# Kernel optimization log

Measured on AMD Instinct MI355X. Metric: run time of the kernel, lower is better.

The kernel has to match this reference:

```python
import jax, jax.numpy as jnp
import numpy as np

PAD_TOKEN_ID = 0
PAGE_SIZE = 64
BOUNDARY_IDS = (13, 30)


def setup_inputs() -> dict:
    B, L, V = 64, 16384, 32000
    P = L // PAGE_SIZE
    key = jax.random.key(0)
    k1, k2, k3 = jax.random.split(key, 3)
    input_ids = jax.random.randint(k1, (B, L), 0, V, dtype=jnp.int32)
    attention_mask = jnp.ones((B, L), dtype=jnp.int32)
    # token -> page index, exactly pos // page_size as SegmentPager would build
    token2page = jnp.broadcast_to(jnp.arange(L, dtype=jnp.int32) // PAGE_SIZE, (B, L))
    keep_pages = jax.random.bernoulli(k2, 0.3, (B, P))  # bool [B, P]
    query_pos = jax.random.randint(k3, (B,), 0, L, dtype=jnp.int32)
    return {
        'input_ids': input_ids,
        'attention_mask': attention_mask,
        'token2page': token2page,
        'keep_pages': keep_pages,
        'query_pos': query_pos,
    }


def reference(input_ids, attention_mask, token2page, keep_pages, query_pos):
    B, L = input_ids.shape
    valid = attention_mask.astype(bool)                         # token_valid [B,L]
    pos = jnp.arange(L, dtype=jnp.int32)

    # --- page-level keep mask gathered per token ---
    t2p = jnp.clip(token2page, 0, None)
    page_keep = jnp.take_along_axis(keep_pages, t2p, axis=1)    # [B,L] bool
    mask = valid & page_keep                                    # keep_token

    # --- force-keep the query tail: mask[qp:] |= valid[qp:] ---
    qp = jnp.clip(query_pos.astype(jnp.int32), 0, L - 1)        # [B]
    tail = pos[None, :] >= qp[:, None]
    mask = mask | (tail & valid)

    # --- sentence rescue in context [0, qp): if any token of a sentence is kept,
    #     keep all valid tokens of that sentence. Sentences are delimited by
    #     boundary tokens (segment = exclusive cumsum of boundary indicators). ---
    boundary = jnp.zeros_like(valid)
    for tid in BOUNDARY_IDS:
        boundary = boundary | (input_ids == tid)
    boundary = boundary & valid
    bcnt = boundary.astype(jnp.int32)
    seg = jnp.cumsum(bcnt, axis=1) - bcnt                       # sentence id per token
    in_ctx = pos[None, :] < qp[:, None]
    seg_d = jnp.where(in_ctx, seg, L)                           # dummy segment L for non-ctx
    flat_seg = (jnp.arange(B, dtype=jnp.int32)[:, None] * (L + 1) + seg_d).reshape(-1)
    keep_any = jax.ops.segment_max(mask.astype(jnp.int32).reshape(-1), flat_seg,
                                   num_segments=B * (L + 1))
    tok_keep = (keep_any[flat_seg] > 0).reshape(B, L)
    mask = mask | (in_ctx & valid & tok_keep)

    # --- fallback: if nothing kept, keep last valid token (or position 0) ---
    any_kept = mask.any(axis=1)
    any_valid = valid.any(axis=1)
    last_valid = jnp.where(any_valid, L - 1 - jnp.argmax(valid[:, ::-1], axis=1), 0)
    fallback = pos[None, :] == last_valid[:, None]
    mask = jnp.where(any_kept[:, None], mask, fallback)

    # --- stream compaction + left-justified padding (padded to L for static shape) ---
    order = jnp.argsort(jnp.logical_not(mask), axis=1)          # stable: kept indices first, in order
    lk = mask.sum(axis=1).astype(jnp.int32)                     # kept length per row
    attn = pos[None, :] < lk[:, None]
    ids_sorted = jnp.take_along_axis(input_ids, order, axis=1)
    ids_comp = jnp.where(attn, ids_sorted, PAD_TOKEN_ID)
    attn_comp = attn.astype(jnp.int32)
    pos_comp = jnp.where(attn, pos[None, :], 0)
    return ids_comp, attn_comp, pos_comp
```

## Files before the change

kernel.cpp:

```cpp
#include <hip/hip_runtime.h>
#include <stdint.h>

#define BB 64
#define LL 16384
#define PP 256
#define WW (LL / 32)
#define NT2 512

__global__ void __launch_bounds__(256) k1_masks(
    const int* __restrict__ g_ids, const int* __restrict__ g_amask,
    const int* __restrict__ g_t2p, const int* __restrict__ g_kp,
    const int* __restrict__ g_qp,
    unsigned* __restrict__ validw, unsigned* __restrict__ bndw,
    unsigned* __restrict__ mask1w)
{
    __shared__ unsigned char kp[PP];
    const int chunk = blockIdx.x;
    const int row   = blockIdx.y;
    const int t     = threadIdx.x;
    if (t < PP) kp[t] = (g_kp[row * PP + t] != 0);
    int qp = g_qp[row];
    qp = qp < 0 ? 0 : (qp > LL - 1 ? LL - 1 : qp);
    __syncthreads();

    const int pos0 = chunk * 2048 + t * 8;
    const int g = row * LL + pos0;
    const int4* idp = (const int4*)(g_ids + g);
    const int4* amp = (const int4*)(g_amask + g);
    const int4* tpp = (const int4*)(g_t2p + g);
    unsigned v8 = 0, b8 = 0, m8 = 0;
#pragma unroll
    for (int jv = 0; jv < 2; ++jv) {
        int4 iv = idp[jv], av = amp[jv], pv = tpp[jv];
        int idsv[4] = {iv.x, iv.y, iv.z, iv.w};
        int amv[4]  = {av.x, av.y, av.z, av.w};
        int tpv[4]  = {pv.x, pv.y, pv.z, pv.w};
#pragma unroll
        for (int k = 0; k < 4; ++k) {
            const int j = jv * 4 + k;
            const int va = (amv[k] != 0);
            const int bd = va && (idsv[k] == 13 || idsv[k] == 30);
            int pg = tpv[k];
            pg = pg < 0 ? 0 : (pg > PP - 1 ? PP - 1 : pg);
            const int m1 = va && (kp[pg] || (pos0 + j) >= qp);
            v8 |= (unsigned)va << j;
            b8 |= (unsigned)bd << j;
            m8 |= (unsigned)m1 << j;
        }
    }
    const int sub = t & 3, sh = 8 * sub;
    unsigned vw = v8 << sh, bw = b8 << sh, mw = m8 << sh;
    vw |= __shfl_xor(vw, 1, 64); vw |= __shfl_xor(vw, 2, 64);
    bw |= __shfl_xor(bw, 1, 64); bw |= __shfl_xor(bw, 2, 64);
    mw |= __shfl_xor(mw, 1, 64); mw |= __shfl_xor(mw, 2, 64);
    if (sub == 0) {
        const int widx = row * WW + chunk * 64 + (t >> 2);
        validw[widx] = vw; bndw[widx] = bw; mask1w[widx] = mw;
    }
}

__device__ __forceinline__ int exscan512(int v, int tid, int* s_wave, int* s_total) {
    __syncthreads();
    const int lane = tid & 63, wv = tid >> 6;
    int inc = v;
#pragma unroll
    for (int off = 1; off < 64; off <<= 1) {
        int n = __shfl_up(inc, off, 64);
        if (lane >= off) inc += n;
    }
    if (lane == 63) s_wave[wv] = inc;
    __syncthreads();
    if (wv == 0) {
        int wval = (lane < 8) ? s_wave[lane] : 0;
        int winc = wval;
#pragma unroll
        for (int off = 1; off < 8; off <<= 1) {
            int n = __shfl_up(winc, off, 64);
            if (lane >= off) winc += n;
        }
        if (lane < 8) s_wave[lane] = winc - wval;
        if (lane == 7) *s_total = winc;
    }
    __syncthreads();
    return inc - v + s_wave[wv];
}

__global__ void __launch_bounds__(NT2) k2_scan(
    const unsigned* __restrict__ validw, const unsigned* __restrict__ bndw,
    const unsigned* __restrict__ mask1w, const int* __restrict__ g_qp,
    unsigned* __restrict__ mask2w, int* __restrict__ wordscan,
    int* __restrict__ lkarr)
{
    __shared__ unsigned segbits[WW];
    __shared__ int s_wave[8];
    __shared__ int s_total;
    __shared__ int s_fb;
    const int row = blockIdx.x;
    const int t = threadIdx.x;
    segbits[t] = 0u;
    int qp = g_qp[row];
    qp = qp < 0 ? 0 : (qp > LL - 1 ? LL - 1 : qp);
    const unsigned vwd = validw[row * WW + t];
    const unsigned bwd = bndw[row * WW + t];
    const unsigned mwd = mask1w[row * WW + t];

    const int segbase = exscan512(__popc(bwd), t, s_wave, &s_total);

    const int rel = qp - t * 32;
    const unsigned ctx = rel <= 0 ? 0u : (rel >= 32 ? 0xFFFFFFFFu : ((1u << rel) - 1u));

    {
        unsigned cands = mwd & ctx;
        if (bwd == 0u) {
            if (cands) {
                const unsigned w_ = (unsigned)segbase >> 5, m_ = 1u << (segbase & 31);
                if ((segbits[w_] & m_) == 0u) atomicOr(&segbits[w_], m_);
            }
        } else {
            while (cands) {
                const int j = __ffs(cands) - 1;
                cands &= cands - 1;
                const int s = segbase + __popc(bwd & ((1u << j) - 1u));
                const unsigned w_ = (unsigned)s >> 5, m_ = 1u << (s & 31);
                if ((segbits[w_] & m_) == 0u) atomicOr(&segbits[w_], m_);
            }
        }
    }
    __syncthreads();

    unsigned m2 = mwd;
    {
        unsigned cand = vwd & ctx & ~mwd;
        if (bwd == 0u) {
            if (cand && ((segbits[(unsigned)segbase >> 5] >> (segbase & 31)) & 1u)) m2 |= cand;
        } else {
            while (cand) {
                const int j = __ffs(cand) - 1;
                cand &= cand - 1;
                const int s = segbase + __popc(bwd & ((1u << j) - 1u));
                if ((segbits[(unsigned)s >> 5] >> (s & 31)) & 1u) m2 |= 1u << j;
            }
        }
    }

    int cb = exscan512(__popc(m2), t, s_wave, &s_total);
    int lk = s_total;

    if (lk == 0) {
        int lastv = vwd ? t * 32 + (31 - __clz(vwd)) : -1;
#pragma unroll
        for (int off = 32; off >= 1; off >>= 1) {
            int n = __shfl_down(lastv, off, 64);
            lastv = lastv > n ? lastv : n;
        }
        __syncthreads();
        if ((t & 63) == 0) s_wave[t >> 6] = lastv;
        __syncthreads();
        if (t == 0) {
            int m = -1;
            for (int w = 0; w < 8; ++w) m = m > s_wave[w] ? m : s_wave[w];
            s_fb = m < 0 ? 0 : m;
        }
        __syncthreads();
        const int fb = s_fb, fw = fb >> 5;
        m2 = (t == fw) ? (1u << (fb & 31)) : 0u;
        cb = (t > fw) ? 1 : 0;
        lk = 1;
    }

    mask2w[row * WW + t] = m2;
    wordscan[row * WW + t] = cb;
    if (t == 0) lkarr[row] = lk;
}

__global__ void __launch_bounds__(256) k3_write(
    const int* __restrict__ g_ids, const unsigned* __restrict__ mask2w,
    const int* __restrict__ wordscan, const int* __restrict__ lkarr,
    int* __restrict__ g_out)
{
    const int chunk = blockIdx.x;
    const int row   = blockIdx.y;
    const int t     = threadIdx.x;
    const int pos0 = chunk * 2048 + t * 8;
    const int widx = row * WW + (pos0 >> 5);
    const unsigned m2 = mask2w[widx];
    const int base = wordscan[widx];
    const int lk = lkarr[row];
    const int sub = t & 3;
    const unsigned mybits = (m2 >> (8 * sub)) & 0xffu;
    const int off = base + __popc(m2 & ((1u << (8 * sub)) - 1u));

    const int g = row * LL + pos0;
    const int4* idp = (const int4*)(g_ids + g);
    int4 i0 = idp[0], i1 = idp[1];

    const int c = row * LL + off;
    if (mybits == 0xffu && (off & 3) == 0) {
        ((int4*)(g_out + c))[0] = i0;
        ((int4*)(g_out + c))[1] = i1;
    } else if (mybits) {
        int idsv[8] = {i0.x, i0.y, i0.z, i0.w, i1.x, i1.y, i1.z, i1.w};
        int cc = c;
        unsigned mm = mybits;
        while (mm) {
            const int j = __ffs(mm) - 1;
            mm &= mm - 1;
            g_out[cc++] = idsv[j];
        }
    }

    if (pos0 + 7 >= lk) {
#pragma unroll
        for (int j = 0; j < 8; ++j)
            if (pos0 + j >= lk) g_out[g + j] = 0;
    }

    int* attn = g_out + (size_t)BB * LL;
    int* pos  = g_out + (size_t)2 * BB * LL;
    int4 a0, a1, p0, p1;
    a0.x = (pos0 + 0) < lk; a0.y = (pos0 + 1) < lk; a0.z = (pos0 + 2) < lk; a0.w = (pos0 + 3) < lk;
    a1.x = (pos0 + 4) < lk; a1.y = (pos0 + 5) < lk; a1.z = (pos0 + 6) < lk; a1.w = (pos0 + 7) < lk;
    p0.x = a0.x ? pos0 + 0 : 0; p0.y = a0.y ? pos0 + 1 : 0; p0.z = a0.z ? pos0 + 2 : 0; p0.w = a0.w ? pos0 + 3 : 0;
    p1.x = a1.x ? pos0 + 4 : 0; p1.y = a1.y ? pos0 + 5 : 0; p1.z = a1.z ? pos0 + 6 : 0; p1.w = a1.w ? pos0 + 7 : 0;
    ((int4*)(attn + g))[0] = a0;
    ((int4*)(attn + g))[1] = a1;
    ((int4*)(pos + g))[0] = p0;
    ((int4*)(pos + g))[1] = p1;
}

extern "C" void kernel_launch(void* const* d_in, const int* in_sizes, int n_in,
                              void* d_out, int out_size, void* d_ws, size_t ws_size,
                              hipStream_t stream) {
    const int* ids = (const int*)d_in[0];
    const int* am  = (const int*)d_in[1];
    const int* t2p = (const int*)d_in[2];
    const int* kpg = (const int*)d_in[3];
    const int* qp  = (const int*)d_in[4];
    int* out       = (int*)d_out;

    unsigned* validw = (unsigned*)d_ws;
    unsigned* bndw   = validw + BB * WW;
    unsigned* mask1w = bndw + BB * WW;
    unsigned* mask2w = mask1w + BB * WW;
    int* wordscan    = (int*)(mask2w + BB * WW);
    int* lkarr       = wordscan + BB * WW;

    dim3 gridA(8, BB);
    k1_masks<<<gridA, 256, 0, stream>>>(ids, am, t2p, kpg, qp, validw, bndw, mask1w);
    k2_scan<<<BB, NT2, 0, stream>>>(validw, bndw, mask1w, qp, mask2w, wordscan, lkarr);
    k3_write<<<gridA, 256, 0, stream>>>(ids, mask2w, wordscan, lkarr, out);
}
```

Before: 83.76 us.

## Fuse three-kernel pipeline into one cooperative kernel with grid syncs

```diff
diff --git a/kernel.cpp b/kernel.cpp
--- a/kernel.cpp
+++ b/kernel.cpp
@@ -1,11 +1,223 @@
 #include <hip/hip_runtime.h>
+#include <hip/hip_cooperative_groups.h>
 #include <stdint.h>
+namespace cg = cooperative_groups;
 
 #define BB 64
 #define LL 16384
 #define PP 256
+#define NCH 8
+#define CHK 2048
+#define NT 256
+#define TPT 8
+#define SEGW 512
 #define WW (LL / 32)
-#define NT2 512
+
+__device__ __forceinline__ int ald(const int* p) {
+    return __hip_atomic_load(p, __ATOMIC_RELAXED, __HIP_MEMORY_SCOPE_AGENT);
+}
+__device__ __forceinline__ void ast(int* p, int v) {
+    __hip_atomic_store(p, v, __ATOMIC_RELAXED, __HIP_MEMORY_SCOPE_AGENT);
+}
+__device__ __forceinline__ unsigned aldu(const unsigned* p) {
+    return __hip_atomic_load(p, __ATOMIC_RELAXED, __HIP_MEMORY_SCOPE_AGENT);
+}
+__device__ __forceinline__ void astu(unsigned* p, unsigned v) {
+    __hip_atomic_store(p, v, __ATOMIC_RELAXED, __HIP_MEMORY_SCOPE_AGENT);
+}
+
+__device__ __forceinline__ int exscan256(int v, int tid, int* s_w, int* s_tot) {
+    __syncthreads();
+    const int lane = tid & 63, wv = tid >> 6;
+    int inc = v;
+#pragma unroll
+    for (int off = 1; off < 64; off <<= 1) {
+        int n = __shfl_up(inc, off, 64);
+        if (lane >= off) inc += n;
+    }
+    if (lane == 63) s_w[wv] = inc;
+    __syncthreads();
+    if (tid == 0) {
+        int t = 0;
+#pragma unroll
+        for (int w = 0; w < 4; ++w) { int u = s_w[w]; s_w[w] = t; t += u; }
+        *s_tot = t;
+    }
+    __syncthreads();
+    return inc - v + s_w[wv];
+}
+
+__global__ void __launch_bounds__(NT) coop_seg(
+    const int* __restrict__ g_ids, const int* __restrict__ g_amask,
+    const int* __restrict__ g_t2p, const int* __restrict__ g_kp,
+    const int* __restrict__ g_qp, int* __restrict__ g_out,
+    unsigned* __restrict__ g_segbits, int* __restrict__ aggr_bnd,
+    int* __restrict__ aggr_kept, int* __restrict__ aggr_lastv)
+{
+    __shared__ unsigned char kp[PP];
+    __shared__ unsigned s_segw[66];
+    __shared__ int s_w[4];
+    __shared__ int s_tot;
+    __shared__ int s_lastv;
+    __shared__ int s_k[NCH];
+    __shared__ int s_l[NCH];
+
+    cg::grid_group gg = cg::this_grid();
+    const int chunk = blockIdx.x;
+    const int row   = blockIdx.y;
+    const int tid   = threadIdx.x;
+    const int bl    = row * NCH + chunk;
+    const int pos0  = chunk * CHK + tid * TPT;
+    const int rowoff = row * LL;
+
+    kp[tid] = (g_kp[row * PP + tid] != 0);
+    if (tid < 64) astu(&g_segbits[bl * 64 + tid], 0u);
+    int qp = g_qp[row];
+    qp = qp < 0 ? 0 : (qp > LL - 1 ? LL - 1 : qp);
+    __syncthreads();
+
+    const int4* idp = (const int4*)(g_ids + rowoff + pos0);
+    const int4* amp = (const int4*)(g_amask + rowoff + pos0);
+    const int4* tpp = (const int4*)(g_t2p + rowoff + pos0);
+    int4 i0 = idp[0], i1 = idp[1];
+    unsigned v8 = 0, b8 = 0, m8 = 0;
+    {
+        int4 a0 = amp[0], a1 = amp[1], p0 = tpp[0], p1 = tpp[1];
+        int idsv[8] = {i0.x, i0.y, i0.z, i0.w, i1.x, i1.y, i1.z, i1.w};
+        int amv[8]  = {a0.x, a0.y, a0.z, a0.w, a1.x, a1.y, a1.z, a1.w};
+        int tpv[8]  = {p0.x, p0.y, p0.z, p0.w, p1.x, p1.y, p1.z, p1.w};
+#pragma unroll
+        for (int j = 0; j < TPT; ++j) {
+            const int va = (amv[j] != 0);
+            const int bd = va && (idsv[j] == 13 || idsv[j] == 30);
+            int pg = tpv[j];
+            pg = pg < 0 ? 0 : (pg > PP - 1 ? PP - 1 : pg);
+            const int m1 = va && (kp[pg] || (pos0 + j) >= qp);
+            v8 |= (unsigned)va << j;
+            b8 |= (unsigned)bd << j;
+            m8 |= (unsigned)m1 << j;
+        }
+    }
+    const int sb_local = exscan256(__popc(b8), tid, s_w, &s_tot);
+    const int bnd_blk = s_tot;
+    if (tid == 0) ast(&aggr_bnd[bl], bnd_blk);
+    gg.sync();
+
+    int chunk_off = 0;
+    for (int c = 0; c < chunk; ++c) chunk_off += ald(&aggr_bnd[row * NCH + c]);
+    const int segb = chunk_off + sb_local;
+    const int w0 = chunk_off >> 5;
+    const int nw = ((chunk_off + bnd_blk) >> 5) - w0 + 1;
+
+    const int rel = qp - pos0;
+    const unsigned ctx = rel <= 0 ? 0u : (rel >= TPT ? 0xFFu : ((1u << rel) - 1u));
+
+    for (int i = tid; i < 66; i += NT) s_segw[i] = 0u;
+    __syncthreads();
+    {
+        unsigned cands = m8 & ctx;
+        while (cands) {
+            const int j = __ffs(cands) - 1;
+            cands &= cands - 1;
+            const int s = segb + __popc(b8 & ((1u << j) - 1u));
+            atomicOr(&s_segw[(s >> 5) - w0], 1u << (s & 31));
+        }
+    }
+    __syncthreads();
+    if (tid < nw) {
+        const unsigned w = s_segw[tid];
+        if (w) atomicOr(&g_segbits[row * SEGW + w0 + tid], w);
+    }
+    gg.sync();
+
+    if (tid < nw) s_segw[tid] = aldu(&g_segbits[row * SEGW + w0 + tid]);
+    if (tid == 0) s_lastv = -1;
+    __syncthreads();
+    unsigned m2 = m8;
+    {
+        unsigned cand = v8 & ctx & ~m8;
+        while (cand) {
+            const int j = __ffs(cand) - 1;
+            cand &= cand - 1;
+            const int s = segb + __popc(b8 & ((1u << j) - 1u));
+            if ((s_segw[(s >> 5) - w0] >> (s & 31)) & 1u) m2 |= 1u << j;
+        }
+    }
+    {
+        const int locallast = v8 ? pos0 + (31 - __clz(v8)) : -1;
+        atomicMax(&s_lastv, locallast);
+    }
+    const int cb_local = exscan256(__popc(m2), tid, s_w, &s_tot);
+    if (tid == 0) {
+        ast(&aggr_kept[bl], s_tot);
+        ast(&aggr_lastv[bl], s_lastv);
+    }
+    gg.sync();
+
+    if (tid < NCH) {
+        s_k[tid] = ald(&aggr_kept[row * NCH + tid]);
+        s_l[tid] = ald(&aggr_lastv[row * NCH + tid]);
+    }
+    __syncthreads();
+    int lk = 0, prefix = 0;
+#pragma unroll
+    for (int c = 0; c < NCH; ++c) {
+        const int k = s_k[c];
+        lk += k;
+        if (c < chunk) prefix += k;
+    }
+    int cbase = prefix + cb_local;
+
+    if (lk == 0) {
+        int fb = -1;
+#pragma unroll
+        for (int c = 0; c < NCH; ++c) fb = fb > s_l[c] ? fb : s_l[c];
+        if (fb < 0) fb = 0;
+        if (chunk == (fb >> 11) && tid == ((fb & (CHK - 1)) >> 3)) {
+            int idsv[8] = {i0.x, i0.y, i0.z, i0.w, i1.x, i1.y, i1.z, i1.w};
+            g_out[rowoff] = idsv[fb & 7];
+        }
+        lk = 1;
+        m2 = 0u;
+    }
+
+    if (m2 == 0xFFu && (cbase & 3) == 0) {
+        ((int4*)(g_out + rowoff + cbase))[0] = i0;
+        ((int4*)(g_out + rowoff + cbase))[1] = i1;
+    } else if (m2) {
+        int idsv[8] = {i0.x, i0.y, i0.z, i0.w, i1.x, i1.y, i1.z, i1.w};
+        int cc = rowoff + cbase;
+        unsigned mm = m2;
+        while (mm) {
+            const int j = __ffs(mm) - 1;
+            mm &= mm - 1;
+            g_out[cc++] = idsv[j];
+        }
+    }
+
+    const int g = rowoff + pos0;
+    if (pos0 >= lk) {
+        int4 z; z.x = z.y = z.z = z.w = 0;
+        ((int4*)(g_out + g))[0] = z;
+        ((int4*)(g_out + g))[1] = z;
+    } else if (pos0 + TPT > lk) {
+#pragma unroll
+        for (int j = 0; j < TPT; ++j)
+            if (pos0 + j >= lk) g_out[g + j] = 0;
+    }
+
+    int* attn = g_out + (size_t)BB * LL;
+    int* pos  = g_out + (size_t)2 * BB * LL;
+    int4 a0, a1, q0, q1;
+    a0.x = (pos0 + 0) < lk; a0.y = (pos0 + 1) < lk; a0.z = (pos0 + 2) < lk; a0.w = (pos0 + 3) < lk;
+    a1.x = (pos0 + 4) < lk; a1.y = (pos0 + 5) < lk; a1.z = (pos0 + 6) < lk; a1.w = (pos0 + 7) < lk;
+    q0.x = a0.x ? pos0 + 0 : 0; q0.y = a0.y ? pos0 + 1 : 0; q0.z = a0.z ? pos0 + 2 : 0; q0.w = a0.w ? pos0 + 3 : 0;
+    q1.x = a1.x ? pos0 + 4 : 0; q1.y = a1.y ? pos0 + 5 : 0; q1.z = a1.z ? pos0 + 6 : 0; q1.w = a1.w ? pos0 + 7 : 0;
+    ((int4*)(attn + g))[0] = a0;
+    ((int4*)(attn + g))[1] = a1;
+    ((int4*)(pos + g))[0] = q0;
+    ((int4*)(pos + g))[1] = q1;
+}
 
 __global__ void __launch_bounds__(256) k1_masks(
     const int* __restrict__ g_ids, const int* __restrict__ g_amask,
@@ -15,14 +227,11 @@
     unsigned* __restrict__ mask1w)
 {
     __shared__ unsigned char kp[PP];
-    const int chunk = blockIdx.x;
-    const int row   = blockIdx.y;
-    const int t     = threadIdx.x;
+    const int chunk = blockIdx.x, row = blockIdx.y, t = threadIdx.x;
     if (t < PP) kp[t] = (g_kp[row * PP + t] != 0);
     int qp = g_qp[row];
     qp = qp < 0 ? 0 : (qp > LL - 1 ? LL - 1 : qp);
     __syncthreads();
-
     const int pos0 = chunk * 2048 + t * 8;
     const int g = row * LL + pos0;
     const int4* idp = (const int4*)(g_ids + g);
@@ -43,9 +252,7 @@
             int pg = tpv[k];
             pg = pg < 0 ? 0 : (pg > PP - 1 ? PP - 1 : pg);
             const int m1 = va && (kp[pg] || (pos0 + j) >= qp);
-            v8 |= (unsigned)va << j;
-            b8 |= (unsigned)bd << j;
-            m8 |= (unsigned)m1 << j;
+            v8 |= (unsigned)va << j; b8 |= (unsigned)bd << j; m8 |= (unsigned)m1 << j;
         }
     }
     const int sub = t & 3, sh = 8 * sub;
@@ -85,7 +292,7 @@
     return inc - v + s_wave[wv];
 }
 
-__global__ void __launch_bounds__(NT2) k2_scan(
+__global__ void __launch_bounds__(512) k2_scan(
     const unsigned* __restrict__ validw, const unsigned* __restrict__ bndw,
     const unsigned* __restrict__ mask1w, const int* __restrict__ g_qp,
     unsigned* __restrict__ mask2w, int* __restrict__ wordscan,
@@ -95,57 +302,39 @@
     __shared__ int s_wave[8];
     __shared__ int s_total;
     __shared__ int s_fb;
-    const int row = blockIdx.x;
-    const int t = threadIdx.x;
+    const int row = blockIdx.x, t = threadIdx.x;
     segbits[t] = 0u;
     int qp = g_qp[row];
     qp = qp < 0 ? 0 : (qp > LL - 1 ? LL - 1 : qp);
     const unsigned vwd = validw[row * WW + t];
     const unsigned bwd = bndw[row * WW + t];
     const unsigned mwd = mask1w[row * WW + t];
-
     const int segbase = exscan512(__popc(bwd), t, s_wave, &s_total);
-
     const int rel = qp - t * 32;
     const unsigned ctx = rel <= 0 ? 0u : (rel >= 32 ? 0xFFFFFFFFu : ((1u << rel) - 1u));
-
     {
         unsigned cands = mwd & ctx;
-        if (bwd == 0u) {
-            if (cands) {
-                const unsigned w_ = (unsigned)segbase >> 5, m_ = 1u << (segbase & 31);
-                if ((segbits[w_] & m_) == 0u) atomicOr(&segbits[w_], m_);
-            }
-        } else {
-            while (cands) {
-                const int j = __ffs(cands) - 1;
-                cands &= cands - 1;
-                const int s = segbase + __popc(bwd & ((1u << j) - 1u));
-                const unsigned w_ = (unsigned)s >> 5, m_ = 1u << (s & 31);
-                if ((segbits[w_] & m_) == 0u) atomicOr(&segbits[w_], m_);
-            }
-        }
-    }
-    __syncthreads();
-
+        while (cands) {
+            const int j = __ffs(cands) - 1;
+            cands &= cands - 1;
+            const int s = segbase + __popc(bwd & ((1u << j) - 1u));
+            const unsigned w_ = (unsigned)s >> 5, m_ = 1u << (s & 31);
+            if ((segbits[w_] & m_) == 0u) atomicOr(&segbits[w_], m_);
+        }
+    }
+    __syncthreads();
     unsigned m2 = mwd;
     {
         unsigned cand = vwd & ctx & ~mwd;
-        if (bwd == 0u) {
-            if (cand && ((segbits[(unsigned)segbase >> 5] >> (segbase & 31)) & 1u)) m2 |= cand;
-        } else {
-            while (cand) {
-                const int j = __ffs(cand) - 1;
-                cand &= cand - 1;
-                const int s = segbase + __popc(bwd & ((1u << j) - 1u));
-                if ((segbits[(unsigned)s >> 5] >> (s & 31)) & 1u) m2 |= 1u << j;
-            }
-        }
-    }
-
+        while (cand) {
+            const int j = __ffs(cand) - 1;
+            cand &= cand - 1;
+            const int s = segbase + __popc(bwd & ((1u << j) - 1u));
+            if ((segbits[(unsigned)s >> 5] >> (s & 31)) & 1u) m2 |= 1u << j;
+        }
+    }
     int cb = exscan512(__popc(m2), t, s_wave, &s_total);
     int lk = s_total;
-
     if (lk == 0) {
         int lastv = vwd ? t * 32 + (31 - __clz(vwd)) : -1;
 #pragma unroll
@@ -167,7 +356,6 @@
         cb = (t > fw) ? 1 : 0;
         lk = 1;
     }
-
     mask2w[row * WW + t] = m2;
     wordscan[row * WW + t] = cb;
     if (t == 0) lkarr[row] = lk;
@@ -178,9 +366,7 @@
     const int* __restrict__ wordscan, const int* __restrict__ lkarr,
     int* __restrict__ g_out)
 {
-    const int chunk = blockIdx.x;
-    const int row   = blockIdx.y;
-    const int t     = threadIdx.x;
+    const int chunk = blockIdx.x, row = blockIdx.y, t = threadIdx.x;
     const int pos0 = chunk * 2048 + t * 8;
     const int widx = row * WW + (pos0 >> 5);
     const unsigned m2 = mask2w[widx];
@@ -189,11 +375,9 @@
     const int sub = t & 3;
     const unsigned mybits = (m2 >> (8 * sub)) & 0xffu;
     const int off = base + __popc(m2 & ((1u << (8 * sub)) - 1u));
-
     const int g = row * LL + pos0;
     const int4* idp = (const int4*)(g_ids + g);
     int4 i0 = idp[0], i1 = idp[1];
-
     const int c = row * LL + off;
     if (mybits == 0xffu && (off & 3) == 0) {
         ((int4*)(g_out + c))[0] = i0;
@@ -208,13 +392,11 @@
             g_out[cc++] = idsv[j];
         }
     }
-
     if (pos0 + 7 >= lk) {
 #pragma unroll
         for (int j = 0; j < 8; ++j)
             if (pos0 + j >= lk) g_out[g + j] = 0;
     }
-
     int* attn = g_out + (size_t)BB * LL;
     int* pos  = g_out + (size_t)2 * BB * LL;
     int4 a0, a1, p0, p1;
@@ -238,15 +420,27 @@
     const int* qp  = (const int*)d_in[4];
     int* out       = (int*)d_out;
 
-    unsigned* validw = (unsigned*)d_ws;
-    unsigned* bndw   = validw + BB * WW;
-    unsigned* mask1w = bndw + BB * WW;
-    unsigned* mask2w = mask1w + BB * WW;
-    int* wordscan    = (int*)(mask2w + BB * WW);
-    int* lkarr       = wordscan + BB * WW;
-
-    dim3 gridA(8, BB);
-    k1_masks<<<gridA, 256, 0, stream>>>(ids, am, t2p, kpg, qp, validw, bndw, mask1w);
-    k2_scan<<<BB, NT2, 0, stream>>>(validw, bndw, mask1w, qp, mask2w, wordscan, lkarr);
-    k3_write<<<gridA, 256, 0, stream>>>(ids, mask2w, wordscan, lkarr, out);
-}
+    unsigned* segbits = (unsigned*)d_ws;
+    int* aggr_bnd   = (int*)(segbits + BB * SEGW);
+    int* aggr_kept  = aggr_bnd + BB * NCH;
+    int* aggr_lastv = aggr_kept + BB * NCH;
+
+    void* args[] = { (void*)&ids, (void*)&am, (void*)&t2p, (void*)&kpg, (void*)&qp,
+                     (void*)&out, (void*)&segbits, (void*)&aggr_bnd,
+                     (void*)&aggr_kept, (void*)&aggr_lastv };
+    hipError_t e = hipLaunchCooperativeKernel((const void*)coop_seg,
+                                              dim3(NCH, BB), dim3(NT),
+                                              args, 0, stream);
+    if (e != hipSuccess) {
+        unsigned* validw = (unsigned*)d_ws;
+        unsigned* bndw   = validw + BB * WW;
+        unsigned* mask1w = bndw + BB * WW;
+        unsigned* mask2w = mask1w + BB * WW;
+        int* wordscan    = (int*)(mask2w + BB * WW);
+        int* lkarr       = wordscan + BB * WW;
+        dim3 gridA(8, BB);
+        k1_masks<<<gridA, 256, 0, stream>>>(ids, am, t2p, kpg, qp, validw, bndw, mask1w);
+        k2_scan<<<BB, 512, 0, stream>>>(validw, bndw, mask1w, qp, mask2w, wordscan, lkarr);
+        k3_write<<<gridA, 256, 0, stream>>>(ids, mask2w, wordscan, lkarr, out);
+    }
+}
```

Result: slower. 243.8 us (+191.1%).

## Fuse three kernels into one with last-arriving block doing the per-row scan

Applied to the files above, without the earlier changes.

```diff
diff --git a/kernel.cpp b/kernel.cpp
--- a/kernel.cpp
+++ b/kernel.cpp
@@ -4,43 +4,91 @@
 #define BB 64
 #define LL 16384
 #define PP 256
+#define NCH 8
+#define CHK 2048
+#define NT 256
+#define TPT 8
 #define WW (LL / 32)
-#define NT2 512
-
-__global__ void __launch_bounds__(256) k1_masks(
+
+__device__ __forceinline__ int ald(const int* p) {
+    return __hip_atomic_load(p, __ATOMIC_RELAXED, __HIP_MEMORY_SCOPE_AGENT);
+}
+__device__ __forceinline__ void ast(int* p, int v) {
+    __hip_atomic_store(p, v, __ATOMIC_RELAXED, __HIP_MEMORY_SCOPE_AGENT);
+}
+__device__ __forceinline__ unsigned aldu(const unsigned* p) {
+    return __hip_atomic_load(p, __ATOMIC_RELAXED, __HIP_MEMORY_SCOPE_AGENT);
+}
+__device__ __forceinline__ void astu(unsigned* p, unsigned v) {
+    __hip_atomic_store(p, v, __ATOMIC_RELAXED, __HIP_MEMORY_SCOPE_AGENT);
+}
+
+__device__ __forceinline__ int exscan256(int v, int tid, int* s_w, int* s_tot) {
+    __syncthreads();
+    const int lane = tid & 63, wv = tid >> 6;
+    int inc = v;
+#pragma unroll
+    for (int off = 1; off < 64; off <<= 1) {
+        int n = __shfl_up(inc, off, 64);
+        if (lane >= off) inc += n;
+    }
+    if (lane == 63) s_w[wv] = inc;
+    __syncthreads();
+    if (tid == 0) {
+        int t = 0;
+#pragma unroll
+        for (int w = 0; w < 4; ++w) { int u = s_w[w]; s_w[w] = t; t += u; }
+        *s_tot = t;
+    }
+    __syncthreads();
+    return inc - v + s_w[wv];
+}
+
+__global__ void __launch_bounds__(64) init_state(int* state) {
+    state[threadIdx.x] = 0;
+}
+
+__global__ void __launch_bounds__(NT, 2) fused_seg(
     const int* __restrict__ g_ids, const int* __restrict__ g_amask,
     const int* __restrict__ g_t2p, const int* __restrict__ g_kp,
-    const int* __restrict__ g_qp,
+    const int* __restrict__ g_qp, int* __restrict__ g_out,
     unsigned* __restrict__ validw, unsigned* __restrict__ bndw,
-    unsigned* __restrict__ mask1w)
+    unsigned* __restrict__ mask1w, unsigned* __restrict__ mask2w,
+    int* __restrict__ wordscan, int* __restrict__ state)
 {
     __shared__ unsigned char kp[PP];
+    __shared__ unsigned s_segw[WW];
+    __shared__ int s_w[4];
+    __shared__ int s_tot;
+    __shared__ int s_master;
+    __shared__ int s_lk;
+
     const int chunk = blockIdx.x;
     const int row   = blockIdx.y;
-    const int t     = threadIdx.x;
-    if (t < PP) kp[t] = (g_kp[row * PP + t] != 0);
+    const int tid   = threadIdx.x;
+    const int rowoff = row * LL;
+    const int pos0 = chunk * CHK + tid * TPT;
+
+    kp[tid] = (g_kp[row * PP + tid] != 0);
     int qp = g_qp[row];
     qp = qp < 0 ? 0 : (qp > LL - 1 ? LL - 1 : qp);
     __syncthreads();
 
-    const int pos0 = chunk * 2048 + t * 8;
-    const int g = row * LL + pos0;
-    const int4* idp = (const int4*)(g_ids + g);
-    const int4* amp = (const int4*)(g_amask + g);
-    const int4* tpp = (const int4*)(g_t2p + g);
+    const int4* idp = (const int4*)(g_ids + rowoff + pos0);
+    const int4* amp = (const int4*)(g_amask + rowoff + pos0);
+    const int4* tpp = (const int4*)(g_t2p + rowoff + pos0);
+    int4 i0 = idp[0], i1 = idp[1];
     unsigned v8 = 0, b8 = 0, m8 = 0;
-#pragma unroll
-    for (int jv = 0; jv < 2; ++jv) {
-        int4 iv = idp[jv], av = amp[jv], pv = tpp[jv];
-        int idsv[4] = {iv.x, iv.y, iv.z, iv.w};
-        int amv[4]  = {av.x, av.y, av.z, av.w};
-        int tpv[4]  = {pv.x, pv.y, pv.z, pv.w};
-#pragma unroll
-        for (int k = 0; k < 4; ++k) {
-            const int j = jv * 4 + k;
-            const int va = (amv[k] != 0);
-            const int bd = va && (idsv[k] == 13 || idsv[k] == 30);
-            int pg = tpv[k];
+    {
+        int4 a0 = amp[0], a1 = amp[1], q0 = tpp[0], q1 = tpp[1];
+        int idsv[8] = {i0.x, i0.y, i0.z, i0.w, i1.x, i1.y, i1.z, i1.w};
+        int amv[8]  = {a0.x, a0.y, a0.z, a0.w, a1.x, a1.y, a1.z, a1.w};
+        int tpv[8]  = {q0.x, q0.y, q0.z, q0.w, q1.x, q1.y, q1.z, q1.w};
+#pragma unroll
+        for (int j = 0; j < TPT; ++j) {
+            const int va = (amv[j] != 0);
+            const int bd = va && (idsv[j] == 13 || idsv[j] == 30);
+            int pg = tpv[j];
             pg = pg < 0 ? 0 : (pg > PP - 1 ? PP - 1 : pg);
             const int m1 = va && (kp[pg] || (pos0 + j) >= qp);
             v8 |= (unsigned)va << j;
@@ -48,159 +96,144 @@
             m8 |= (unsigned)m1 << j;
         }
     }
-    const int sub = t & 3, sh = 8 * sub;
-    unsigned vw = v8 << sh, bw = b8 << sh, mw = m8 << sh;
-    vw |= __shfl_xor(vw, 1, 64); vw |= __shfl_xor(vw, 2, 64);
-    bw |= __shfl_xor(bw, 1, 64); bw |= __shfl_xor(bw, 2, 64);
-    mw |= __shfl_xor(mw, 1, 64); mw |= __shfl_xor(mw, 2, 64);
-    if (sub == 0) {
-        const int widx = row * WW + chunk * 64 + (t >> 2);
-        validw[widx] = vw; bndw[widx] = bw; mask1w[widx] = mw;
-    }
-}
-
-__device__ __forceinline__ int exscan512(int v, int tid, int* s_wave, int* s_total) {
-    __syncthreads();
-    const int lane = tid & 63, wv = tid >> 6;
-    int inc = v;
-#pragma unroll
-    for (int off = 1; off < 64; off <<= 1) {
-        int n = __shfl_up(inc, off, 64);
-        if (lane >= off) inc += n;
-    }
-    if (lane == 63) s_wave[wv] = inc;
-    __syncthreads();
-    if (wv == 0) {
-        int wval = (lane < 8) ? s_wave[lane] : 0;
-        int winc = wval;
-#pragma unroll
-        for (int off = 1; off < 8; off <<= 1) {
-            int n = __shfl_up(winc, off, 64);
-            if (lane >= off) winc += n;
-        }
-        if (lane < 8) s_wave[lane] = winc - wval;
-        if (lane == 7) *s_total = winc;
-    }
-    __syncthreads();
-    return inc - v + s_wave[wv];
-}
-
-__global__ void __launch_bounds__(NT2) k2_scan(
-    const unsigned* __restrict__ validw, const unsigned* __restrict__ bndw,
-    const unsigned* __restrict__ mask1w, const int* __restrict__ g_qp,
-    unsigned* __restrict__ mask2w, int* __restrict__ wordscan,
-    int* __restrict__ lkarr)
-{
-    __shared__ unsigned segbits[WW];
-    __shared__ int s_wave[8];
-    __shared__ int s_total;
-    __shared__ int s_fb;
-    const int row = blockIdx.x;
-    const int t = threadIdx.x;
-    segbits[t] = 0u;
-    int qp = g_qp[row];
-    qp = qp < 0 ? 0 : (qp > LL - 1 ? LL - 1 : qp);
-    const unsigned vwd = validw[row * WW + t];
-    const unsigned bwd = bndw[row * WW + t];
-    const unsigned mwd = mask1w[row * WW + t];
-
-    const int segbase = exscan512(__popc(bwd), t, s_wave, &s_total);
-
-    const int rel = qp - t * 32;
-    const unsigned ctx = rel <= 0 ? 0u : (rel >= 32 ? 0xFFFFFFFFu : ((1u << rel) - 1u));
-
     {
-        unsigned cands = mwd & ctx;
-        if (bwd == 0u) {
-            if (cands) {
-                const unsigned w_ = (unsigned)segbase >> 5, m_ = 1u << (segbase & 31);
-                if ((segbits[w_] & m_) == 0u) atomicOr(&segbits[w_], m_);
-            }
-        } else {
-            while (cands) {
-                const int j = __ffs(cands) - 1;
-                cands &= cands - 1;
-                const int s = segbase + __popc(bwd & ((1u << j) - 1u));
-                const unsigned w_ = (unsigned)s >> 5, m_ = 1u << (s & 31);
-                if ((segbits[w_] & m_) == 0u) atomicOr(&segbits[w_], m_);
-            }
-        }
-    }
-    __syncthreads();
-
-    unsigned m2 = mwd;
-    {
-        unsigned cand = vwd & ctx & ~mwd;
-        if (bwd == 0u) {
-            if (cand && ((segbits[(unsigned)segbase >> 5] >> (segbase & 31)) & 1u)) m2 |= cand;
-        } else {
-            while (cand) {
-                const int j = __ffs(cand) - 1;
-                cand &= cand - 1;
-                const int s = segbase + __popc(bwd & ((1u << j) - 1u));
-                if ((segbits[(unsigned)s >> 5] >> (s & 31)) & 1u) m2 |= 1u << j;
-            }
-        }
-    }
-
-    int cb = exscan512(__popc(m2), t, s_wave, &s_total);
-    int lk = s_total;
-
-    if (lk == 0) {
-        int lastv = vwd ? t * 32 + (31 - __clz(vwd)) : -1;
-#pragma unroll
-        for (int off = 32; off >= 1; off >>= 1) {
-            int n = __shfl_down(lastv, off, 64);
-            lastv = lastv > n ? lastv : n;
+        const int sub = tid & 3, sh = 8 * sub;
+        unsigned vw = v8 << sh, bw = b8 << sh, mw = m8 << sh;
+        vw |= __shfl_xor(vw, 1, 64); vw |= __shfl_xor(vw, 2, 64);
+        bw |= __shfl_xor(bw, 1, 64); bw |= __shfl_xor(bw, 2, 64);
+        mw |= __shfl_xor(mw, 1, 64); mw |= __shfl_xor(mw, 2, 64);
+        if (sub == 0) {
+            const int widx = row * WW + chunk * 64 + (tid >> 2);
+            astu(&validw[widx], vw); astu(&bndw[widx], bw); astu(&mask1w[widx], mw);
+        }
+    }
+    __syncthreads();
+    if (tid == 0)
+        s_master = __hip_atomic_fetch_add(&state[row], 1, __ATOMIC_ACQ_REL,
+                                          __HIP_MEMORY_SCOPE_AGENT);
+    __syncthreads();
+    const bool master = (s_master == 7);
+
+    int lk;
+    if (master) {
+        const int w0i = 2 * tid, w1i = 2 * tid + 1;
+        const int base_idx = row * WW;
+        const unsigned bw0 = aldu(&bndw[base_idx + w0i]);
+        const unsigned bw1 = aldu(&bndw[base_idx + w1i]);
+        const unsigned vw0 = aldu(&validw[base_idx + w0i]);
+        const unsigned vw1 = aldu(&validw[base_idx + w1i]);
+        const unsigned mw0 = aldu(&mask1w[base_idx + w0i]);
+        const unsigned mw1 = aldu(&mask1w[base_idx + w1i]);
+        s_segw[w0i] = 0u; s_segw[w1i] = 0u;
+
+        const int sb0 = exscan256(__popc(bw0) + __popc(bw1), tid, s_w, &s_tot);
+        const int sb1 = sb0 + __popc(bw0);
+
+        const int rel0 = qp - w0i * 32, rel1 = qp - w1i * 32;
+        const unsigned ctx0 = rel0 <= 0 ? 0u : (rel0 >= 32 ? 0xFFFFFFFFu : ((1u << rel0) - 1u));
+        const unsigned ctx1 = rel1 <= 0 ? 0u : (rel1 >= 32 ? 0xFFFFFFFFu : ((1u << rel1) - 1u));
+
+#pragma unroll
+        for (int h = 0; h < 2; ++h) {
+            const unsigned bw_ = h ? bw1 : bw0;
+            unsigned cands = h ? (mw1 & ctx1) : (mw0 & ctx0);
+            const int sb_ = h ? sb1 : sb0;
+            if (bw_ == 0u) {
+                if (cands) {
+                    const unsigned w_ = (unsigned)sb_ >> 5, m_ = 1u << (sb_ & 31);
+                    if ((s_segw[w_] & m_) == 0u) atomicOr(&s_segw[w_], m_);
+                }
+            } else {
+                while (cands) {
+                    const int j = __ffs(cands) - 1;
+                    cands &= cands - 1;
+                    const int s = sb_ + __popc(bw_ & ((1u << j) - 1u));
+                    const unsigned w_ = (unsigned)s >> 5, m_ = 1u << (s & 31);
+                    if ((s_segw[w_] & m_) == 0u) atomicOr(&s_segw[w_], m_);
+                }
+            }
         }
         __syncthreads();
-        if ((t & 63) == 0) s_wave[t >> 6] = lastv;
+
+        unsigned m2w0 = mw0, m2w1 = mw1;
+#pragma unroll
+        for (int h = 0; h < 2; ++h) {
+            const unsigned bw_ = h ? bw1 : bw0;
+            unsigned cand = h ? (vw1 & ctx1 & ~mw1) : (vw0 & ctx0 & ~mw0);
+            const int sb_ = h ? sb1 : sb0;
+            unsigned add = 0u;
+            if (bw_ == 0u) {
+                if (cand && ((s_segw[(unsigned)sb_ >> 5] >> (sb_ & 31)) & 1u)) add = cand;
+            } else {
+                while (cand) {
+                    const int j = __ffs(cand) - 1;
+                    cand &= cand - 1;
+                    const int s = sb_ + __popc(bw_ & ((1u << j) - 1u));
+                    if ((s_segw[(unsigned)s >> 5] >> (s & 31)) & 1u) add |= 1u << j;
+                }
+            }
+            if (h) m2w1 |= add; else m2w0 |= add;
+        }
+
+        int cb = exscan256(__popc(m2w0) + __popc(m2w1), tid, s_w, &s_tot);
+        lk = s_tot;
+
+        if (lk == 0) {
+            int lv = vw1 ? w1i * 32 + (31 - __clz(vw1))
+                         : (vw0 ? w0i * 32 + (31 - __clz(vw0)) : -1);
+#pragma unroll
+            for (int off = 32; off >= 1; off >>= 1) {
+                int n = __shfl_down(lv, off, 64);
+                lv = lv > n ? lv : n;
+            }
+            __syncthreads();
+            if ((tid & 63) == 0) s_w[tid >> 6] = lv;
+            __syncthreads();
+            if (tid == 0) {
+                int m = -1;
+#pragma unroll
+                for (int w = 0; w < 4; ++w) m = m > s_w[w] ? m : s_w[w];
+                const int fb = m < 0 ? 0 : m;
+                g_out[rowoff] = g_ids[rowoff + fb];
+            }
+            m2w0 = 0u; m2w1 = 0u; cb = 0; lk = 1;
+        }
+
+        astu(&mask2w[base_idx + w0i], m2w0);
+        astu(&mask2w[base_idx + w1i], m2w1);
+        ast(&wordscan[base_idx + w0i], cb);
+        ast(&wordscan[base_idx + w1i], cb + __popc(m2w0));
+        if (tid == 0) s_lk = lk;
         __syncthreads();
-        if (t == 0) {
-            int m = -1;
-            for (int w = 0; w < 8; ++w) m = m > s_wave[w] ? m : s_wave[w];
-            s_fb = m < 0 ? 0 : m;
+        if (tid == 0)
+            __hip_atomic_fetch_add(&state[row], (1 << 4) | (lk << 5),
+                                   __ATOMIC_ACQ_REL, __HIP_MEMORY_SCOPE_AGENT);
+        lk = s_lk;
+    } else {
+        if (tid == 0) {
+            int s;
+            while ((((s = __hip_atomic_load(&state[row], __ATOMIC_RELAXED,
+                                            __HIP_MEMORY_SCOPE_AGENT)) >> 4) & 1) == 0)
+                __builtin_amdgcn_s_sleep(16);
+            s_lk = s >> 5;
         }
         __syncthreads();
-        const int fb = s_fb, fw = fb >> 5;
-        m2 = (t == fw) ? (1u << (fb & 31)) : 0u;
-        cb = (t > fw) ? 1 : 0;
-        lk = 1;
-    }
-
-    mask2w[row * WW + t] = m2;
-    wordscan[row * WW + t] = cb;
-    if (t == 0) lkarr[row] = lk;
-}
-
-__global__ void __launch_bounds__(256) k3_write(
-    const int* __restrict__ g_ids, const unsigned* __restrict__ mask2w,
-    const int* __restrict__ wordscan, const int* __restrict__ lkarr,
-    int* __restrict__ g_out)
-{
-    const int chunk = blockIdx.x;
-    const int row   = blockIdx.y;
-    const int t     = threadIdx.x;
-    const int pos0 = chunk * 2048 + t * 8;
-    const int widx = row * WW + (pos0 >> 5);
-    const unsigned m2 = mask2w[widx];
-    const int base = wordscan[widx];
-    const int lk = lkarr[row];
-    const int sub = t & 3;
+        lk = s_lk;
+    }
+
+    const int widx = row * WW + chunk * 64 + (tid >> 2);
+    const unsigned m2 = aldu(&mask2w[widx]);
+    const int wbase = ald(&wordscan[widx]);
+    const int sub = tid & 3;
     const unsigned mybits = (m2 >> (8 * sub)) & 0xffu;
-    const int off = base + __popc(m2 & ((1u << (8 * sub)) - 1u));
-
-    const int g = row * LL + pos0;
-    const int4* idp = (const int4*)(g_ids + g);
-    int4 i0 = idp[0], i1 = idp[1];
-
-    const int c = row * LL + off;
+    const int off = wbase + __popc(m2 & ((1u << (8 * sub)) - 1u));
+
     if (mybits == 0xffu && (off & 3) == 0) {
-        ((int4*)(g_out + c))[0] = i0;
-        ((int4*)(g_out + c))[1] = i1;
+        ((int4*)(g_out + rowoff + off))[0] = i0;
+        ((int4*)(g_out + rowoff + off))[1] = i1;
     } else if (mybits) {
         int idsv[8] = {i0.x, i0.y, i0.z, i0.w, i1.x, i1.y, i1.z, i1.w};
-        int cc = c;
+        int cc = rowoff + off;
         unsigned mm = mybits;
         while (mm) {
             const int j = __ffs(mm) - 1;
@@ -209,23 +242,28 @@
         }
     }
 
-    if (pos0 + 7 >= lk) {
-#pragma unroll
-        for (int j = 0; j < 8; ++j)
+    const int g = rowoff + pos0;
+    if (pos0 >= lk) {
+        int4 z; z.x = z.y = z.z = z.w = 0;
+        ((int4*)(g_out + g))[0] = z;
+        ((int4*)(g_out + g))[1] = z;
+    } else if (pos0 + TPT > lk) {
+#pragma unroll
+        for (int j = 0; j < TPT; ++j)
             if (pos0 + j >= lk) g_out[g + j] = 0;
     }
 
     int* attn = g_out + (size_t)BB * LL;
     int* pos  = g_out + (size_t)2 * BB * LL;
-    int4 a0, a1, p0, p1;
+    int4 a0, a1, q0, q1;
     a0.x = (pos0 + 0) < lk; a0.y = (pos0 + 1) < lk; a0.z = (pos0 + 2) < lk; a0.w = (pos0 + 3) < lk;
     a1.x = (pos0 + 4) < lk; a1.y = (pos0 + 5) < lk; a1.z = (pos0 + 6) < lk; a1.w = (pos0 + 7) < lk;
-    p0.x = a0.x ? pos0 + 0 : 0; p0.y = a0.y ? pos0 + 1 : 0; p0.z = a0.z ? pos0 + 2 : 0; p0.w = a0.w ? pos0 + 3 : 0;
-    p1.x = a1.x ? pos0 + 4 : 0; p1.y = a1.y ? pos0 + 5 : 0; p1.z = a1.z ? pos0 + 6 : 0; p1.w = a1.w ? pos0 + 7 : 0;
+    q0.x = a0.x ? pos0 + 0 : 0; q0.y = a0.y ? pos0 + 1 : 0; q0.z = a0.z ? pos0 + 2 : 0; q0.w = a0.w ? pos0 + 3 : 0;
+    q1.x = a1.x ? pos0 + 4 : 0; q1.y = a1.y ? pos0 + 5 : 0; q1.z = a1.z ? pos0 + 6 : 0; q1.w = a1.w ? pos0 + 7 : 0;
     ((int4*)(attn + g))[0] = a0;
     ((int4*)(attn + g))[1] = a1;
-    ((int4*)(pos + g))[0] = p0;
-    ((int4*)(pos + g))[1] = p1;
+    ((int4*)(pos + g))[0] = q0;
+    ((int4*)(pos + g))[1] = q1;
 }
 
 extern "C" void kernel_launch(void* const* d_in, const int* in_sizes, int n_in,
@@ -243,10 +281,10 @@
     unsigned* mask1w = bndw + BB * WW;
     unsigned* mask2w = mask1w + BB * WW;
     int* wordscan    = (int*)(mask2w + BB * WW);
-    int* lkarr       = wordscan + BB * WW;
-
-    dim3 gridA(8, BB);
-    k1_masks<<<gridA, 256, 0, stream>>>(ids, am, t2p, kpg, qp, validw, bndw, mask1w);
-    k2_scan<<<BB, NT2, 0, stream>>>(validw, bndw, mask1w, qp, mask2w, wordscan, lkarr);
-    k3_write<<<gridA, 256, 0, stream>>>(ids, mask2w, wordscan, lkarr, out);
-}
+    int* state       = wordscan + BB * WW;
+
+    init_state<<<1, 64, 0, stream>>>(state);
+    fused_seg<<<dim3(NCH, BB), NT, 0, stream>>>(ids, am, t2p, kpg, qp, out,
+                                                validw, bndw, mask1w, mask2w,
+                                                wordscan, state);
+}
```

Result: slower. 95.41 us (+13.9%).
